# Kernel optimization log

Hardware: AMD Instinct MI355X
Metric: run time of the kernel (lower is better)

The kernel has to match this reference:

```python
import jax, jax.numpy as jnp
import numpy as np

B_, L_, D_MODEL = 4, 2048, 1024
D_STATE, EXPAND, D_CONV = 16, 2, 4
D_INNER = EXPAND * D_MODEL          # 2048
DT_RANK = (D_MODEL + 15) // 16      # 64 (mamba default: ceil(d_model/16))
EPS = 1e-6


def setup_inputs() -> dict:
    key = jax.random.key(0)
    ks = jax.random.split(key, 12)
    s = 0.02
    x = jax.random.normal(ks[0], (B_, L_, D_MODEL), dtype=jnp.float32)
    c = jax.random.normal(ks[1], (B_, D_MODEL), dtype=jnp.float32)
    W_in = jax.random.normal(ks[2], (D_MODEL, 2 * D_INNER), dtype=jnp.float32) * s
    conv_w = jax.random.normal(ks[3], (D_INNER, D_CONV), dtype=jnp.float32) * s
    conv_b = jnp.zeros((D_INNER,), dtype=jnp.float32)
    W_xproj = jax.random.normal(ks[4], (D_INNER, DT_RANK + 2 * D_STATE), dtype=jnp.float32) * s
    W_dt = jax.random.normal(ks[5], (DT_RANK, D_INNER), dtype=jnp.float32) * s
    # dt bias so softplus(dt) starts in a reasonable range (~0.001..0.1)
    dt = jnp.exp(jax.random.uniform(ks[6], (D_INNER,)) * (np.log(0.1) - np.log(0.001)) + np.log(0.001))
    b_dt = (dt + jnp.log(-jnp.expm1(-dt))).astype(jnp.float32)  # inverse softplus
    # A = repeat(1..d_state) per channel (mamba S4D-real init)
    A_log = jnp.log(jnp.tile(jnp.arange(1, D_STATE + 1, dtype=jnp.float32)[None, :], (D_INNER, 1)))
    D_skip = jnp.ones((D_INNER,), dtype=jnp.float32)
    W_out = jax.random.normal(ks[7], (D_INNER, D_MODEL), dtype=jnp.float32) * s
    W_ada = jax.random.normal(ks[8], (D_MODEL, 3 * D_MODEL), dtype=jnp.float32) * s
    b_ada = jnp.zeros((3 * D_MODEL,), dtype=jnp.float32)
    return dict(x=x, c=c, W_in=W_in, conv_w=conv_w, conv_b=conv_b,
                W_xproj=W_xproj, W_dt=W_dt, b_dt=b_dt, A_log=A_log,
                D_skip=D_skip, W_out=W_out, W_ada=W_ada, b_ada=b_ada)


def _mamba(x, W_in, conv_w, conv_b, W_xproj, W_dt, b_dt, A_log, D_skip, W_out):
    Bb, L, _ = x.shape
    xm, z = jnp.split(x @ W_in, 2, axis=-1)            # each [B, L, d_inner]
    # causal depthwise conv, kernel D_CONV
    xp = jnp.pad(xm, ((0, 0), (D_CONV - 1, 0), (0, 0)))
    xc = conv_b + sum(xp[:, k:k + L, :] * conv_w[:, k] for k in range(D_CONV))
    xc = jax.nn.silu(xc)                               # u: [B, L, d_inner]
    dbc = xc @ W_xproj
    dt, Bs, Cs = jnp.split(dbc, [DT_RANK, DT_RANK + D_STATE], axis=-1)
    delta = jax.nn.softplus(dt @ W_dt + b_dt)          # [B, L, d_inner]
    A = -jnp.exp(A_log)                                # [d_inner, d_state]

    def step(h, inp):
        d_t, B_t, C_t, u_t = inp                       # [B,di], [B,s], [B,s], [B,di]
        dA = jnp.exp(d_t[..., None] * A)               # [B, di, s]
        h = dA * h + (d_t * u_t)[..., None] * B_t[:, None, :]
        y = jnp.einsum('bds,bs->bd', h, C_t)
        return h, y

    xs = (jnp.moveaxis(delta, 1, 0), jnp.moveaxis(Bs, 1, 0),
          jnp.moveaxis(Cs, 1, 0), jnp.moveaxis(xc, 1, 0))
    h0 = jnp.zeros((Bb, D_INNER, D_STATE), dtype=x.dtype)
    _, ys = jax.lax.scan(step, h0, xs)
    y = jnp.moveaxis(ys, 0, 1) + xc * D_skip
    y = y * jax.nn.silu(z)
    return y @ W_out


def reference(x, c, W_in, conv_w, conv_b, W_xproj, W_dt, b_dt, A_log, D_skip, W_out, W_ada, b_ada):
    mod = jax.nn.silu(c) @ W_ada + b_ada
    scale, shift, gate = jnp.split(mod, 3, axis=-1)    # each [B, d_model]
    residual = x
    mu = x.mean(-1, keepdims=True)
    var = x.var(-1, keepdims=True)
    xn = (x - mu) * jax.lax.rsqrt(var + EPS)           # LayerNorm, no affine
    h = xn * (1.0 + scale[:, None, :]) + shift[:, None, :]
    out = _mamba(h, W_in, conv_w, conv_b, W_xproj, W_dt, b_dt, A_log, D_skip, W_out)
    return residual + gate[:, None, :] * out
```

## Files before the change

### kernel.cpp

```cpp
#include <hip/hip_runtime.h>
#include <hip/hip_bf16.h>
#include <stdint.h>


#define L_ 2048
#define DM 1024
#define DI 2048
#define DS 16
#define NC 32
#define TC 64

typedef __bf16 bf16x8 __attribute__((ext_vector_type(8)));
typedef float f32x4 __attribute__((ext_vector_type(4)));

__device__ __forceinline__ float bf2f(unsigned int u) {
  union { unsigned int i; float f; } c;
  c.i = (u & 0xFFFFu) << 16;
  return c.f;
}
__device__ __forceinline__ unsigned short f2bf(float f) {
  union { float f; unsigned int i; } c; c.f = f;
  unsigned int x = c.i;
  return (unsigned short)((x + 0x7FFFu + ((x >> 16) & 1u)) >> 16);
}
__device__ __forceinline__ float silu_f(float v) { return v / (1.f + __expf(-v)); }

__device__ __forceinline__ void async_cp16(unsigned short* lds, const unsigned short* g) {
  __builtin_amdgcn_global_load_lds(
      (const __attribute__((address_space(1))) unsigned int*)g,
      (__attribute__((address_space(3))) unsigned int*)lds, 16, 0, 0);
}

__global__ __launch_bounds__(256) void k_wt4(const float* __restrict__ s0, unsigned short* __restrict__ d0,
                                             const float* __restrict__ s1, unsigned short* __restrict__ d1,
                                             const float* __restrict__ s2, unsigned short* __restrict__ d2,
                                             const float* __restrict__ s3, unsigned short* __restrict__ d3) {
  int bid = blockIdx.x;
  const float* src; unsigned short* dst; int K, N, NP, kb, nb;
  if (bid < 4096)                { src = s0; dst = d0; K = 1024; N = 4096; NP = 4096; kb = bid & 31; nb = bid >> 5; }
  else if ((bid -= 4096) < 2048) { src = s1; dst = d1; K = 2048; N = 1024; NP = 1024; kb = bid & 63; nb = bid >> 6; }
  else if ((bid -= 2048) < 256)  { src = s2; dst = d2; K = 2048; N = 96;   NP = 128;  kb = bid & 63; nb = bid >> 6; }
  else { bid -= 256;               src = s3; dst = d3; K = 64;   N = 2048; NP = 2048; kb = bid & 1;  nb = bid >> 1; }
  __shared__ float tile[32][33];
  const int kb0 = kb * 32, nb0 = nb * 32;
  const int tx = threadIdx.x & 31, ty = threadIdx.x >> 5;
#pragma unroll
  for (int i = 0; i < 4; i++) {
    int k = kb0 + ty + 8 * i, n = nb0 + tx;
    float v = 0.f;
    if (k < K && n < N) v = src[(size_t)k * N + n];
    tile[ty + 8 * i][tx] = v;
  }
  __syncthreads();
#pragma unroll
  for (int i = 0; i < 4; i++) {
    int n = nb0 + ty + 8 * i, k = kb0 + tx;
    if (n < NP && k < K) dst[(size_t)n * K + k] = f2bf(tile[tx][ty + 8 * i]);
  }
}

__global__ __launch_bounds__(256) void k_ada(const float* __restrict__ c,
                                             const float* __restrict__ W,
                                             const float* __restrict__ bias,
                                             float* __restrict__ mod) {
  __shared__ float sc[DM];
  const int b = blockIdx.y, tid = threadIdx.x;
  for (int k = tid; k < DM; k += 256) sc[k] = silu_f(c[b * DM + k]);
  __syncthreads();
  const int j = blockIdx.x * 256 + tid;
  float acc = bias[j];
#pragma unroll 8
  for (int k = 0; k < DM; k++) acc += sc[k] * W[(size_t)k * 3072 + j];
  mod[b * 3072 + j] = acc;
}

__global__ __launch_bounds__(256) void k_ln(const float* __restrict__ x,
                                            const float* __restrict__ mod,
                                            unsigned short* __restrict__ h) {
  const int row = blockIdx.x, b = row >> 11, tid = threadIdx.x;
  const float4 v = ((const float4*)(x + (size_t)row * DM))[tid];
  float s = v.x + v.y + v.z + v.w;
  float ss = v.x * v.x + v.y * v.y + v.z * v.z + v.w * v.w;
#pragma unroll
  for (int off = 32; off; off >>= 1) { s += __shfl_down(s, off); ss += __shfl_down(ss, off); }
  __shared__ float red[10];
  const int wv = tid >> 6, ln = tid & 63;
  if (ln == 0) { red[wv] = s; red[4 + wv] = ss; }
  __syncthreads();
  if (tid == 0) {
    float st = red[0] + red[1] + red[2] + red[3];
    float sst = red[4] + red[5] + red[6] + red[7];
    float mu = st * (1.f / DM);
    red[8] = mu;
    red[9] = rsqrtf(sst * (1.f / DM) - mu * mu + 1e-6f);
  }
  __syncthreads();
  const float mu = red[8], rstd = red[9];
  const int ccol = tid * 4;
  const float4 sc = *(const float4*)(mod + b * 3072 + ccol);
  const float4 sh = *(const float4*)(mod + b * 3072 + DM + ccol);
  uint2 p;
  p.x = (unsigned)f2bf((v.x - mu) * rstd * (1.f + sc.x) + sh.x) |
        ((unsigned)f2bf((v.y - mu) * rstd * (1.f + sc.y) + sh.y) << 16);
  p.y = (unsigned)f2bf((v.z - mu) * rstd * (1.f + sc.z) + sh.z) |
        ((unsigned)f2bf((v.w - mu) * rstd * (1.f + sc.w) + sh.w) << 16);
  *(uint2*)(h + (size_t)row * DM + ccol) = p;
}

struct GArgs {
  const unsigned short* A;
  const unsigned short* Bt;
  int lda, ldb, klen;
  float* f0;
  unsigned short* h0;
  unsigned short* h1;
  const float* c0;
  const float* c1;
};

template<int EPI>
__global__ __launch_bounds__(256, 2) void k_gemm(GArgs g) {
  __shared__ unsigned short sA[128 * 32];
  __shared__ unsigned short sB[128 * 32];
  const int tid = threadIdx.x;
  const int w = tid >> 6, lane = tid & 63;
  const int m0 = blockIdx.x * 128, n0 = blockIdx.y * 128;
  const int kstart = blockIdx.z * g.klen;
  const int r4 = lane >> 2;
  const int c8 = (lane & 3) * 8;
  const int rowA0 = w * 16 + r4, rowA1 = (w + 4) * 16 + r4;
  const unsigned short* gA0 = g.A + (size_t)(m0 + rowA0) * g.lda + kstart + c8;
  const unsigned short* gA1 = g.A + (size_t)(m0 + rowA1) * g.lda + kstart + c8;
  const unsigned short* gB0 = g.Bt + (size_t)(n0 + rowA0) * g.ldb + kstart + c8;
  const unsigned short* gB1 = g.Bt + (size_t)(n0 + rowA1) * g.ldb + kstart + c8;
  unsigned short* lA0 = sA + w * 512;
  unsigned short* lA1 = sA + (w + 4) * 512;
  unsigned short* lB0 = sB + w * 512;
  unsigned short* lB1 = sB + (w + 4) * 512;
  const int mw = (w & 1) * 64, nw = (w >> 1) * 64;
  const int row16 = lane & 15, k8 = (lane >> 4) * 8;
  f32x4 acc[4][4] = {};
  for (int kk = 0; kk < g.klen; kk += 32) {
    async_cp16(lA0, gA0); async_cp16(lA1, gA1);
    async_cp16(lB0, gB0); async_cp16(lB1, gB1);
    gA0 += 32; gA1 += 32; gB0 += 32; gB1 += 32;
    __syncthreads();
    bf16x8 av[4], bv[4];
#pragma unroll
    for (int i = 0; i < 4; i++)
      av[i] = *(const bf16x8*)(sA + (mw + 16 * i + row16) * 32 + k8);
#pragma unroll
    for (int j = 0; j < 4; j++)
      bv[j] = *(const bf16x8*)(sB + (nw + 16 * j + row16) * 32 + k8);
#pragma unroll
    for (int i = 0; i < 4; i++)
#pragma unroll
      for (int j = 0; j < 4; j++)
        acc[i][j] = __builtin_amdgcn_mfma_f32_16x16x32_bf16(av[i], bv[j], acc[i][j], 0, 0, 0);
    __syncthreads();
  }
  const int qr = (lane >> 4) * 4, cn = lane & 15;
#pragma unroll
  for (int i = 0; i < 4; i++) {
    const int m = m0 + mw + 16 * i + qr;
    const int b = m >> 11;
#pragma unroll
    for (int j = 0; j < 4; j++) {
      const int n = n0 + nw + 16 * j + cn;
      f32x4 v = acc[i][j];
      if constexpr (EPI == 0) {
#pragma unroll
        for (int r = 0; r < 4; r++) {
          unsigned short* dst = (n < DI)
              ? g.h0 + (size_t)(m + r) * DI + n
              : g.h1 + (size_t)(m + r) * DI + (n - DI);
          *dst = f2bf(v[r]);
        }
      } else if constexpr (EPI == 1) {
        *(f32x4*)(g.f0 + ((size_t)(blockIdx.z * 128 + n)) * 8192 + m) = v;
      } else if constexpr (EPI == 2) {
        const float bn = g.c0[n];
#pragma unroll
        for (int r = 0; r < 4; r++) {
          float xx = v[r] + bn;
          g.h0[(size_t)(m + r) * DI + n] = f2bf((xx > 15.f) ? xx : __logf(1.f + __expf(xx)));
        }
      } else {
        const float gate = g.c1[b * 3072 + 2048 + n];
#pragma unroll
        for (int r = 0; r < 4; r++) {
          size_t idx = (size_t)(m + r) * DM + n;
          g.f0[idx] = g.c0[idx] + gate * v[r];
        }
      }
    }
  }
}

__global__ __launch_bounds__(256) void k_conv(const unsigned short* __restrict__ xm,
                                              const float* __restrict__ conv_w,
                                              const float* __restrict__ conv_b,
                                              unsigned short* __restrict__ u) {
  const int b = blockIdx.z;
  const int t = blockIdx.x * 32 + (threadIdx.x >> 3);
  const int d = blockIdx.y * 64 + (threadIdx.x & 7) * 8;
  const size_t rowbase = ((size_t)(b * L_ + t)) * DI + d;
  uint4 r3 = *(const uint4*)(xm + rowbase);
  uint4 r0 = make_uint4(0, 0, 0, 0), r1 = r0, r2 = r0;
  if (t >= 3) r0 = *(const uint4*)(xm + rowbase - 3 * DI);
  if (t >= 2) r1 = *(const uint4*)(xm + rowbase - 2 * DI);
  if (t >= 1) r2 = *(const uint4*)(xm + rowbase - 1 * DI);
  float x0[8], x1[8], x2[8], x3[8];
  const unsigned* p0 = (const unsigned*)&r0;
  const unsigned* p1 = (const unsigned*)&r1;
  const unsigned* p2 = (const unsigned*)&r2;
  const unsigned* p3 = (const unsigned*)&r3;
#pragma unroll
  for (int q = 0; q < 4; q++) {
    x0[2 * q] = bf2f(p0[q]); x0[2 * q + 1] = bf2f(p0[q] >> 16);
    x1[2 * q] = bf2f(p1[q]); x1[2 * q + 1] = bf2f(p1[q] >> 16);
    x2[2 * q] = bf2f(p2[q]); x2[2 * q + 1] = bf2f(p2[q] >> 16);
    x3[2 * q] = bf2f(p3[q]); x3[2 * q + 1] = bf2f(p3[q] >> 16);
  }
  const f32x4 cb0 = *(const f32x4*)(conv_b + d);
  const f32x4 cb1 = *(const f32x4*)(conv_b + d + 4);
  unsigned out[4];
#pragma unroll
  for (int j = 0; j < 8; j++) {
    const f32x4 wj = *(const f32x4*)(conv_w + (size_t)(d + j) * 4);
    const float cb = (j < 4) ? cb0[j] : cb1[j - 4];
    float a = cb + wj[0] * x0[j] + wj[1] * x1[j] + wj[2] * x2[j] + wj[3] * x3[j];
    unsigned short us = f2bf(silu_f(a));
    if (j & 1) out[j >> 1] |= ((unsigned)us << 16);
    else out[j >> 1] = us;
  }
  *(uint4*)(u + rowbase) = make_uint4(out[0], out[1], out[2], out[3]);
}

__global__ __launch_bounds__(256) void k_xsplit(const float* __restrict__ pt,
                                                unsigned short* __restrict__ dtb,
                                                float* __restrict__ BC) {
  const int bx = blockIdx.x;
  const int n = bx >> 5;
  const int m = ((bx & 31) << 8) + threadIdx.x;
  float v = pt[(size_t)n * 8192 + m] + pt[(size_t)(128 + n) * 8192 + m] +
            pt[(size_t)(256 + n) * 8192 + m] + pt[(size_t)(384 + n) * 8192 + m];
  if (n < 64) dtb[(size_t)m * 64 + n] = f2bf(v);
  else if (n < 80) BC[(size_t)m * 32 + (n - 64)] = v;
  else BC[(size_t)m * 32 + 16 + (n - 80)] = v;
}

__global__ __launch_bounds__(256, 4) void k_scanA(const unsigned short* __restrict__ delta,
                                                  const unsigned short* __restrict__ u,
                                                  const float* __restrict__ BC,
                                                  const float* __restrict__ A_log,
                                                  float* __restrict__ hloc,
                                                  float* __restrict__ dsum) {
  const int b = blockIdx.y, c = blockIdx.z;
  const int d = blockIdx.x * 256 + threadIdx.x;
  const size_t mbase = (size_t)(b * L_ + c * TC);
  const unsigned short* dp = delta + mbase * DI + d;
  const unsigned short* up = u + mbase * DI + d;
  const float* bc = BC + mbase * 32;
  float As[16];
#pragma unroll
  for (int q = 0; q < 4; q++) {
    const f32x4 av = *(const f32x4*)(A_log + (size_t)d * 16 + q * 4);
#pragma unroll
    for (int j = 0; j < 4; j++) As[q * 4 + j] = -__expf(av[j]);
  }
  float h[16];
#pragma unroll
  for (int s = 0; s < 16; s++) h[s] = 0.f;
  float sd = 0.f;
  for (int t8 = 0; t8 < TC; t8 += 8) {
    float dv[8], uvf[8];
#pragma unroll
    for (int i = 0; i < 8; i++) dv[i] = bf2f(dp[(size_t)(t8 + i) * DI]);
#pragma unroll
    for (int i = 0; i < 8; i++) uvf[i] = bf2f(up[(size_t)(t8 + i) * DI]);
#pragma unroll
    for (int i = 0; i < 8; i++) {
      const float dvi = dv[i];
      const float w = dvi * uvf[i];
      sd += dvi;
      const float* bct = bc + (size_t)(t8 + i) * 32;
#pragma unroll
      for (int q = 0; q < 4; q++) {
        const f32x4 bq = *(const f32x4*)(bct + q * 4);
#pragma unroll
        for (int j = 0; j < 4; j++) {
          const int s = q * 4 + j;
          const float a = __expf(dvi * As[s]);
          h[s] = a * h[s] + w * bq[j];
        }
      }
    }
  }
  float* hl = hloc + (((size_t)(b * NC + c)) * DI + d) * 16;
#pragma unroll
  for (int q = 0; q < 4; q++) {
    f32x4 v = {h[q * 4], h[q * 4 + 1], h[q * 4 + 2], h[q * 4 + 3]};
    *(f32x4*)(hl + q * 4) = v;
  }
  dsum[((size_t)(b * NC + c)) * DI + d] = sd;
}

__global__ __launch_bounds__(256) void k_scanB(const float* __restrict__ hloc,
                                               const float* __restrict__ dsum,
                                               const float* __restrict__ A_log,
                                               float* __restrict__ hin) {
  const int i = blockIdx.x * 256 + threadIdx.x;
  const int b = i >> 11, d = i & 2047;
  float As[16];
#pragma unroll
  for (int q = 0; q < 4; q++) {
    const f32x4 av = *(const f32x4*)(A_log + (size_t)d * 16 + q * 4);
#pragma unroll
    for (int j = 0; j < 4; j++) As[q * 4 + j] = -__expf(av[j]);
  }
  float H[16];
#pragma unroll
  for (int s = 0; s < 16; s++) H[s] = 0.f;
  for (int c = 0; c < NC; c++) {
    float* hp = hin + (((size_t)(b * NC + c)) * DI + d) * 16;
#pragma unroll
    for (int q = 0; q < 4; q++) {
      f32x4 v = {H[q * 4], H[q * 4 + 1], H[q * 4 + 2], H[q * 4 + 3]};
      *(f32x4*)(hp + q * 4) = v;
    }
    if (c < NC - 1) {
      const float sd = dsum[((size_t)(b * NC + c)) * DI + d];
      const float* hl = hloc + (((size_t)(b * NC + c)) * DI + d) * 16;
#pragma unroll
      for (int s = 0; s < 16; s++)
        H[s] = __expf(sd * As[s]) * H[s] + hl[s];
    }
  }
}

__global__ __launch_bounds__(256, 4) void k_scanC(const unsigned short* __restrict__ delta,
                                                  const unsigned short* __restrict__ u,
                                                  const unsigned short* __restrict__ z,
                                                  const float* __restrict__ BC,
                                                  const float* __restrict__ A_log,
                                                  const float* __restrict__ Dsk,
                                                  const float* __restrict__ hin,
                                                  unsigned short* __restrict__ y) {
  const int b = blockIdx.y, c = blockIdx.z;
  const int d = blockIdx.x * 256 + threadIdx.x;
  const size_t mbase = (size_t)(b * L_ + c * TC);
  const unsigned short* dp = delta + mbase * DI + d;
  const unsigned short* up = u + mbase * DI + d;
  const unsigned short* zp = z + mbase * DI + d;
  const float* bc = BC + mbase * 32;
  float As[16];
#pragma unroll
  for (int q = 0; q < 4; q++) {
    const f32x4 av = *(const f32x4*)(A_log + (size_t)d * 16 + q * 4);
#pragma unroll
    for (int j = 0; j < 4; j++) As[q * 4 + j] = -__expf(av[j]);
  }
  const float dsk = Dsk[d];
  float h[16];
  const float* hp = hin + (((size_t)(b * NC + c)) * DI + d) * 16;
#pragma unroll
  for (int q = 0; q < 4; q++) {
    const f32x4 v = *(const f32x4*)(hp + q * 4);
#pragma unroll
    for (int j = 0; j < 4; j++) h[q * 4 + j] = v[j];
  }
  unsigned short* yp = y + mbase * DI + d;
  for (int t8 = 0; t8 < TC; t8 += 8) {
    float dv[8], uvf[8], zvf[8];
#pragma unroll
    for (int i = 0; i < 8; i++) dv[i] = bf2f(dp[(size_t)(t8 + i) * DI]);
#pragma unroll
    for (int i = 0; i < 8; i++) uvf[i] = bf2f(up[(size_t)(t8 + i) * DI]);
#pragma unroll
    for (int i = 0; i < 8; i++) zvf[i] = bf2f(zp[(size_t)(t8 + i) * DI]);
#pragma unroll
    for (int i = 0; i < 8; i++) {
      const float dvi = dv[i];
      const float w = dvi * uvf[i];
      const float* bct = bc + (size_t)(t8 + i) * 32;
      float y0 = 0.f, y1 = 0.f;
#pragma unroll
      for (int q = 0; q < 4; q++) {
        const f32x4 bq = *(const f32x4*)(bct + q * 4);
        const f32x4 cq = *(const f32x4*)(bct + 16 + q * 4);
#pragma unroll
        for (int j = 0; j < 4; j++) {
          const int s = q * 4 + j;
          const float a = __expf(dvi * As[s]);
          h[s] = a * h[s] + w * bq[j];
          if (j & 1) y1 += h[s] * cq[j]; else y0 += h[s] * cq[j];
        }
      }
      const float yt = (y0 + y1 + uvf[i] * dsk) * silu_f(zvf[i]);
      yp[(size_t)(t8 + i) * DI] = f2bf(yt);
    }
  }
}

extern "C" void kernel_launch(void* const* d_in, const int* in_sizes, int n_in,
                              void* d_out, int out_size, void* d_ws, size_t ws_size,
                              hipStream_t stream) {
  const float* x      = (const float*)d_in[0];
  const float* c      = (const float*)d_in[1];
  const float* W_in   = (const float*)d_in[2];
  const float* conv_w = (const float*)d_in[3];
  const float* conv_b = (const float*)d_in[4];
  const float* W_xp   = (const float*)d_in[5];
  const float* W_dt   = (const float*)d_in[6];
  const float* b_dt   = (const float*)d_in[7];
  const float* A_log  = (const float*)d_in[8];
  const float* D_skip = (const float*)d_in[9];
  const float* W_out  = (const float*)d_in[10];
  const float* W_ada  = (const float*)d_in[11];
  const float* b_ada  = (const float*)d_in[12];
  float* out = (float*)d_out;

  char* ws = (char*)d_ws;
  size_t off = 0;
  auto take = [&](size_t bytes) {
    char* p = ws + off;
    off += (bytes + 255) & ~(size_t)255;
    return p;
  };
  float* mod             = (float*)take((size_t)4 * 3072 * 4);
  unsigned short* Wt_in  = (unsigned short*)take((size_t)4096 * 1024 * 2);
  unsigned short* Wt_out = (unsigned short*)take((size_t)1024 * 2048 * 2);
  unsigned short* Wt_xp  = (unsigned short*)take((size_t)128 * 2048 * 2);
  unsigned short* Wt_dt  = (unsigned short*)take((size_t)2048 * 64 * 2);
  unsigned short* h_bf   = (unsigned short*)take((size_t)8192 * 1024 * 2);
  unsigned short* xm     = (unsigned short*)take((size_t)4 * 2048 * 2048 * 2);
  unsigned short* z_bf   = (unsigned short*)take((size_t)4 * 2048 * 2048 * 2);
  unsigned short* scanws = (unsigned short*)take((size_t)4 * 2048 * 2048 * 2);
  unsigned short* u_bf   = (unsigned short*)take((size_t)8192 * 2048 * 2);
  unsigned short* delta  = (unsigned short*)take((size_t)8192 * 2048 * 2);
  unsigned short* dt_bf  = (unsigned short*)take((size_t)8192 * 64 * 2);
  float* BC              = (float*)take((size_t)4 * 2048 * 32 * 4);
  float* part_T = (float*)h_bf;
  float* hin    = (float*)h_bf;
  float* hloc   = (float*)scanws;
  float* dsum   = (float*)(scanws + (size_t)8 * 1024 * 1024);
  unsigned short* y_bf = xm;

  k_wt4<<<6528, 256, 0, stream>>>(W_in, Wt_in, W_out, Wt_out, W_xp, Wt_xp, W_dt, Wt_dt);
  k_ada<<<dim3(12, 4), 256, 0, stream>>>(c, W_ada, b_ada, mod);
  k_ln<<<8192, 256, 0, stream>>>(x, mod, h_bf);
  GArgs a1{h_bf, Wt_in, 1024, 1024, 1024, nullptr, xm, z_bf, nullptr, nullptr};
  k_gemm<0><<<dim3(64, 32), 256, 0, stream>>>(a1);
  k_conv<<<dim3(64, 32, 4), 256, 0, stream>>>(xm, conv_w, conv_b, u_bf);
  GArgs a2{u_bf, Wt_xp, 2048, 2048, 512, part_T, nullptr, nullptr, nullptr, nullptr};
  k_gemm<1><<<dim3(64, 1, 4), 256, 0, stream>>>(a2);
  k_xsplit<<<3072, 256, 0, stream>>>(part_T, dt_bf, BC);
  GArgs a3{dt_bf, Wt_dt, 64, 64, 64, nullptr, delta, nullptr, b_dt, nullptr};
  k_gemm<2><<<dim3(64, 16), 256, 0, stream>>>(a3);
  k_scanA<<<dim3(8, 4, NC - 1), 256, 0, stream>>>(delta, u_bf, BC, A_log, hloc, dsum);
  k_scanB<<<32, 256, 0, stream>>>(hloc, dsum, A_log, hin);
  k_scanC<<<dim3(8, 4, NC), 256, 0, stream>>>(delta, u_bf, z_bf, BC, A_log, D_skip, hin, y_bf);
  GArgs a4{y_bf, Wt_out, 2048, 2048, 2048, out, nullptr, nullptr, x, mod};
  k_gemm<3><<<dim3(64, 8), 256, 0, stream>>>(a4);
}
```

Measured before the change: 587.5 us.

## Replace per-state exps in scan with a power chain when A is arithmetic

```diff
diff --git a/kernel.cpp b/kernel.cpp
--- a/kernel.cpp
+++ b/kernel.cpp
@@ -25,25 +25,66 @@
 }
 __device__ __forceinline__ float silu_f(float v) { return v / (1.f + __expf(-v)); }
 
+__device__ __forceinline__ void pow_chain(float a1, float* p) {
+  p[0] = a1;
+#pragma unroll
+  for (int s = 1; s < 16; s++) p[s] = p[(s - 1) >> 1] * p[s >> 1];
+}
+
 __device__ __forceinline__ void async_cp16(unsigned short* lds, const unsigned short* g) {
   __builtin_amdgcn_global_load_lds(
       (const __attribute__((address_space(1))) unsigned int*)g,
       (__attribute__((address_space(3))) unsigned int*)lds, 16, 0, 0);
 }
 
-__global__ __launch_bounds__(256) void k_wt4(const float* __restrict__ s0, unsigned short* __restrict__ d0,
+__global__ __launch_bounds__(256) void k_chk(const float* __restrict__ A_log,
+                                             int* __restrict__ flag) {
+  __shared__ int ok;
+  if (threadIdx.x == 0) ok = 1;
+  __syncthreads();
+  int good = 1;
+  for (int i = threadIdx.x; i < DI * DS; i += 256) {
+    const int s = i & 15, d = i >> 4;
+    const float a = __expf(A_log[i]);
+    const float expect = __expf(A_log[d * 16]) * (float)(s + 1);
+    if (fabsf(a - expect) > 1e-4f * expect) good = 0;
+  }
+  if (!good) atomicAnd(&ok, 0);
+  __syncthreads();
+  if (threadIdx.x == 0) flag[0] = ok;
+}
+
+__global__ __launch_bounds__(256) void k_pre(const float* __restrict__ s0, unsigned short* __restrict__ d0,
                                              const float* __restrict__ s1, unsigned short* __restrict__ d1,
                                              const float* __restrict__ s2, unsigned short* __restrict__ d2,
-                                             const float* __restrict__ s3, unsigned short* __restrict__ d3) {
+                                             const float* __restrict__ s3, unsigned short* __restrict__ d3,
+                                             const float* __restrict__ cvec,
+                                             const float* __restrict__ W_ada,
+                                             const float* __restrict__ b_ada,
+                                             float* __restrict__ mod) {
+  __shared__ float tile[32][33];
   int bid = blockIdx.x;
+  const int tid = threadIdx.x;
+  if (bid >= 6528) {
+    bid -= 6528;
+    const int b = bid / 12, jb = bid % 12;
+    float* sc = &tile[0][0];
+    for (int k = tid; k < DM; k += 256) sc[k] = silu_f(cvec[b * DM + k]);
+    __syncthreads();
+    const int j = jb * 256 + tid;
+    float acc = b_ada[j];
+#pragma unroll 8
+    for (int k = 0; k < DM; k++) acc += sc[k] * W_ada[(size_t)k * 3072 + j];
+    mod[b * 3072 + j] = acc;
+    return;
+  }
   const float* src; unsigned short* dst; int K, N, NP, kb, nb;
   if (bid < 4096)                { src = s0; dst = d0; K = 1024; N = 4096; NP = 4096; kb = bid & 31; nb = bid >> 5; }
   else if ((bid -= 4096) < 2048) { src = s1; dst = d1; K = 2048; N = 1024; NP = 1024; kb = bid & 63; nb = bid >> 6; }
   else if ((bid -= 2048) < 256)  { src = s2; dst = d2; K = 2048; N = 96;   NP = 128;  kb = bid & 63; nb = bid >> 6; }
   else { bid -= 256;               src = s3; dst = d3; K = 64;   N = 2048; NP = 2048; kb = bid & 1;  nb = bid >> 1; }
-  __shared__ float tile[32][33];
   const int kb0 = kb * 32, nb0 = nb * 32;
-  const int tx = threadIdx.x & 31, ty = threadIdx.x >> 5;
+  const int tx = tid & 31, ty = tid >> 5;
 #pragma unroll
   for (int i = 0; i < 4; i++) {
     int k = kb0 + ty + 8 * i, n = nb0 + tx;
@@ -57,21 +98,6 @@
     int n = nb0 + ty + 8 * i, k = kb0 + tx;
     if (n < NP && k < K) dst[(size_t)n * K + k] = f2bf(tile[tx][ty + 8 * i]);
   }
-}
-
-__global__ __launch_bounds__(256) void k_ada(const float* __restrict__ c,
-                                             const float* __restrict__ W,
-                                             const float* __restrict__ bias,
-                                             float* __restrict__ mod) {
-  __shared__ float sc[DM];
-  const int b = blockIdx.y, tid = threadIdx.x;
-  for (int k = tid; k < DM; k += 256) sc[k] = silu_f(c[b * DM + k]);
-  __syncthreads();
-  const int j = blockIdx.x * 256 + tid;
-  float acc = bias[j];
-#pragma unroll 8
-  for (int k = 0; k < DM; k++) acc += sc[k] * W[(size_t)k * 3072 + j];
-  mod[b * 3072 + j] = acc;
 }
 
 __global__ __launch_bounds__(256) void k_ln(const float* __restrict__ x,
@@ -254,45 +280,75 @@
                                                   const unsigned short* __restrict__ u,
                                                   const float* __restrict__ BC,
                                                   const float* __restrict__ A_log,
+                                                  const int* __restrict__ flag,
                                                   float* __restrict__ hloc,
                                                   float* __restrict__ dsum) {
   const int b = blockIdx.y, c = blockIdx.z;
   const int d = blockIdx.x * 256 + threadIdx.x;
+  const int fast = flag[0];
   const size_t mbase = (size_t)(b * L_ + c * TC);
   const unsigned short* dp = delta + mbase * DI + d;
   const unsigned short* up = u + mbase * DI + d;
   const float* bc = BC + mbase * 32;
-  float As[16];
-#pragma unroll
-  for (int q = 0; q < 4; q++) {
-    const f32x4 av = *(const f32x4*)(A_log + (size_t)d * 16 + q * 4);
-#pragma unroll
-    for (int j = 0; j < 4; j++) As[q * 4 + j] = -__expf(av[j]);
-  }
   float h[16];
 #pragma unroll
   for (int s = 0; s < 16; s++) h[s] = 0.f;
   float sd = 0.f;
-  for (int t8 = 0; t8 < TC; t8 += 8) {
-    float dv[8], uvf[8];
-#pragma unroll
-    for (int i = 0; i < 8; i++) dv[i] = bf2f(dp[(size_t)(t8 + i) * DI]);
-#pragma unroll
-    for (int i = 0; i < 8; i++) uvf[i] = bf2f(up[(size_t)(t8 + i) * DI]);
-#pragma unroll
-    for (int i = 0; i < 8; i++) {
-      const float dvi = dv[i];
-      const float w = dvi * uvf[i];
-      sd += dvi;
-      const float* bct = bc + (size_t)(t8 + i) * 32;
-#pragma unroll
-      for (int q = 0; q < 4; q++) {
-        const f32x4 bq = *(const f32x4*)(bct + q * 4);
-#pragma unroll
-        for (int j = 0; j < 4; j++) {
-          const int s = q * 4 + j;
-          const float a = __expf(dvi * As[s]);
-          h[s] = a * h[s] + w * bq[j];
+  if (fast) {
+    const float As0 = -__expf(A_log[(size_t)d * 16]);
+    for (int t8 = 0; t8 < TC; t8 += 8) {
+      float dv[8], uvf[8];
+#pragma unroll
+      for (int i = 0; i < 8; i++) dv[i] = bf2f(dp[(size_t)(t8 + i) * DI]);
+#pragma unroll
+      for (int i = 0; i < 8; i++) uvf[i] = bf2f(up[(size_t)(t8 + i) * DI]);
+#pragma unroll
+      for (int i = 0; i < 8; i++) {
+        const float dvi = dv[i];
+        const float w = dvi * uvf[i];
+        sd += dvi;
+        const float* bct = bc + (size_t)(t8 + i) * 32;
+        float p[16];
+        pow_chain(__expf(dvi * As0), p);
+#pragma unroll
+        for (int q = 0; q < 4; q++) {
+          const f32x4 bq = *(const f32x4*)(bct + q * 4);
+#pragma unroll
+          for (int j = 0; j < 4; j++) {
+            const int s = q * 4 + j;
+            h[s] = p[s] * h[s] + w * bq[j];
+          }
+        }
+      }
+    }
+  } else {
+    float As[16];
+#pragma unroll
+    for (int q = 0; q < 4; q++) {
+      const f32x4 av = *(const f32x4*)(A_log + (size_t)d * 16 + q * 4);
+#pragma unroll
+      for (int j = 0; j < 4; j++) As[q * 4 + j] = -__expf(av[j]);
+    }
+    for (int t8 = 0; t8 < TC; t8 += 8) {
+      float dv[8], uvf[8];
+#pragma unroll
+      for (int i = 0; i < 8; i++) dv[i] = bf2f(dp[(size_t)(t8 + i) * DI]);
+#pragma unroll
+      for (int i = 0; i < 8; i++) uvf[i] = bf2f(up[(size_t)(t8 + i) * DI]);
+#pragma unroll
+      for (int i = 0; i < 8; i++) {
+        const float dvi = dv[i];
+        const float w = dvi * uvf[i];
+        sd += dvi;
+        const float* bct = bc + (size_t)(t8 + i) * 32;
+#pragma unroll
+        for (int q = 0; q < 4; q++) {
+          const f32x4 bq = *(const f32x4*)(bct + q * 4);
+#pragma unroll
+          for (int j = 0; j < 4; j++) {
+            const int s = q * 4 + j;
+            h[s] = __expf(dvi * As[s]) * h[s] + w * bq[j];
+          }
         }
       }
     }
@@ -309,15 +365,20 @@
 __global__ __launch_bounds__(256) void k_scanB(const float* __restrict__ hloc,
                                                const float* __restrict__ dsum,
                                                const float* __restrict__ A_log,
+                                               const int* __restrict__ flag,
                                                float* __restrict__ hin) {
   const int i = blockIdx.x * 256 + threadIdx.x;
   const int b = i >> 11, d = i & 2047;
+  const int fast = flag[0];
   float As[16];
-#pragma unroll
-  for (int q = 0; q < 4; q++) {
-    const f32x4 av = *(const f32x4*)(A_log + (size_t)d * 16 + q * 4);
-#pragma unroll
-    for (int j = 0; j < 4; j++) As[q * 4 + j] = -__expf(av[j]);
+  const float As0 = -__expf(A_log[(size_t)d * 16]);
+  if (!fast) {
+#pragma unroll
+    for (int q = 0; q < 4; q++) {
+      const f32x4 av = *(const f32x4*)(A_log + (size_t)d * 16 + q * 4);
+#pragma unroll
+      for (int j = 0; j < 4; j++) As[q * 4 + j] = -__expf(av[j]);
+    }
   }
   float H[16];
 #pragma unroll
@@ -332,9 +393,15 @@
     if (c < NC - 1) {
       const float sd = dsum[((size_t)(b * NC + c)) * DI + d];
       const float* hl = hloc + (((size_t)(b * NC + c)) * DI + d) * 16;
-#pragma unroll
-      for (int s = 0; s < 16; s++)
-        H[s] = __expf(sd * As[s]) * H[s] + hl[s];
+      if (fast) {
+        float p[16];
+        pow_chain(__expf(sd * As0), p);
+#pragma unroll
+        for (int s = 0; s < 16; s++) H[s] = p[s] * H[s] + hl[s];
+      } else {
+#pragma unroll
+        for (int s = 0; s < 16; s++) H[s] = __expf(sd * As[s]) * H[s] + hl[s];
+      }
     }
   }
 }
@@ -345,22 +412,17 @@
                                                   const float* __restrict__ BC,
                                                   const float* __restrict__ A_log,
                                                   const float* __restrict__ Dsk,
+                                                  const int* __restrict__ flag,
                                                   const float* __restrict__ hin,
                                                   unsigned short* __restrict__ y) {
   const int b = blockIdx.y, c = blockIdx.z;
   const int d = blockIdx.x * 256 + threadIdx.x;
+  const int fast = flag[0];
   const size_t mbase = (size_t)(b * L_ + c * TC);
   const unsigned short* dp = delta + mbase * DI + d;
   const unsigned short* up = u + mbase * DI + d;
   const unsigned short* zp = z + mbase * DI + d;
   const float* bc = BC + mbase * 32;
-  float As[16];
-#pragma unroll
-  for (int q = 0; q < 4; q++) {
-    const f32x4 av = *(const f32x4*)(A_log + (size_t)d * 16 + q * 4);
-#pragma unroll
-    for (int j = 0; j < 4; j++) As[q * 4 + j] = -__expf(av[j]);
-  }
   const float dsk = Dsk[d];
   float h[16];
   const float* hp = hin + (((size_t)(b * NC + c)) * DI + d) * 16;
@@ -371,34 +433,75 @@
     for (int j = 0; j < 4; j++) h[q * 4 + j] = v[j];
   }
   unsigned short* yp = y + mbase * DI + d;
-  for (int t8 = 0; t8 < TC; t8 += 8) {
-    float dv[8], uvf[8], zvf[8];
-#pragma unroll
-    for (int i = 0; i < 8; i++) dv[i] = bf2f(dp[(size_t)(t8 + i) * DI]);
-#pragma unroll
-    for (int i = 0; i < 8; i++) uvf[i] = bf2f(up[(size_t)(t8 + i) * DI]);
-#pragma unroll
-    for (int i = 0; i < 8; i++) zvf[i] = bf2f(zp[(size_t)(t8 + i) * DI]);
-#pragma unroll
-    for (int i = 0; i < 8; i++) {
-      const float dvi = dv[i];
-      const float w = dvi * uvf[i];
-      const float* bct = bc + (size_t)(t8 + i) * 32;
-      float y0 = 0.f, y1 = 0.f;
-#pragma unroll
-      for (int q = 0; q < 4; q++) {
-        const f32x4 bq = *(const f32x4*)(bct + q * 4);
-        const f32x4 cq = *(const f32x4*)(bct + 16 + q * 4);
-#pragma unroll
-        for (int j = 0; j < 4; j++) {
-          const int s = q * 4 + j;
-          const float a = __expf(dvi * As[s]);
-          h[s] = a * h[s] + w * bq[j];
-          if (j & 1) y1 += h[s] * cq[j]; else y0 += h[s] * cq[j];
-        }
+  if (fast) {
+    const float As0 = -__expf(A_log[(size_t)d * 16]);
+    for (int t8 = 0; t8 < TC; t8 += 8) {
+      float dv[8], uvf[8], zvf[8];
+#pragma unroll
+      for (int i = 0; i < 8; i++) dv[i] = bf2f(dp[(size_t)(t8 + i) * DI]);
+#pragma unroll
+      for (int i = 0; i < 8; i++) uvf[i] = bf2f(up[(size_t)(t8 + i) * DI]);
+#pragma unroll
+      for (int i = 0; i < 8; i++) zvf[i] = bf2f(zp[(size_t)(t8 + i) * DI]);
+#pragma unroll
+      for (int i = 0; i < 8; i++) {
+        const float dvi = dv[i];
+        const float w = dvi * uvf[i];
+        const float* bct = bc + (size_t)(t8 + i) * 32;
+        float p[16];
+        pow_chain(__expf(dvi * As0), p);
+        float y0 = 0.f, y1 = 0.f;
+#pragma unroll
+        for (int q = 0; q < 4; q++) {
+          const f32x4 bq = *(const f32x4*)(bct + q * 4);
+          const f32x4 cq = *(const f32x4*)(bct + 16 + q * 4);
+#pragma unroll
+          for (int j = 0; j < 4; j++) {
+            const int s = q * 4 + j;
+            h[s] = p[s] * h[s] + w * bq[j];
+            if (j & 1) y1 += h[s] * cq[j]; else y0 += h[s] * cq[j];
+          }
+        }
+        const float yt = (y0 + y1 + uvf[i] * dsk) * silu_f(zvf[i]);
+        yp[(size_t)(t8 + i) * DI] = f2bf(yt);
       }
-      const float yt = (y0 + y1 + uvf[i] * dsk) * silu_f(zvf[i]);
-      yp[(size_t)(t8 + i) * DI] = f2bf(yt);
+    }
+  } else {
+    float As[16];
+#pragma unroll
+    for (int q = 0; q < 4; q++) {
+      const f32x4 av = *(const f32x4*)(A_log + (size_t)d * 16 + q * 4);
+#pragma unroll
+      for (int j = 0; j < 4; j++) As[q * 4 + j] = -__expf(av[j]);
+    }
+    for (int t8 = 0; t8 < TC; t8 += 8) {
+      float dv[8], uvf[8], zvf[8];
+#pragma unroll
+      for (int i = 0; i < 8; i++) dv[i] = bf2f(dp[(size_t)(t8 + i) * DI]);
+#pragma unroll
+      for (int i = 0; i < 8; i++) uvf[i] = bf2f(up[(size_t)(t8 + i) * DI]);
+#pragma unroll
+      for (int i = 0; i < 8; i++) zvf[i] = bf2f(zp[(size_t)(t8 + i) * DI]);
+#pragma unroll
+      for (int i = 0; i < 8; i++) {
+        const float dvi = dv[i];
+        const float w = dvi * uvf[i];
+        const float* bct = bc + (size_t)(t8 + i) * 32;
+        float y0 = 0.f, y1 = 0.f;
+#pragma unroll
+        for (int q = 0; q < 4; q++) {
+          const f32x4 bq = *(const f32x4*)(bct + q * 4);
+          const f32x4 cq = *(const f32x4*)(bct + 16 + q * 4);
+#pragma unroll
+          for (int j = 0; j < 4; j++) {
+            const int s = q * 4 + j;
+            h[s] = __expf(dvi * As[s]) * h[s] + w * bq[j];
+            if (j & 1) y1 += h[s] * cq[j]; else y0 += h[s] * cq[j];
+          }
+        }
+        const float yt = (y0 + y1 + uvf[i] * dsk) * silu_f(zvf[i]);
+        yp[(size_t)(t8 + i) * DI] = f2bf(yt);
+      }
     }
   }
 }
@@ -441,14 +544,16 @@
   unsigned short* delta  = (unsigned short*)take((size_t)8192 * 2048 * 2);
   unsigned short* dt_bf  = (unsigned short*)take((size_t)8192 * 64 * 2);
   float* BC              = (float*)take((size_t)4 * 2048 * 32 * 4);
+  int* flag              = (int*)take(256);
   float* part_T = (float*)h_bf;
   float* hin    = (float*)h_bf;
   float* hloc   = (float*)scanws;
   float* dsum   = (float*)(scanws + (size_t)8 * 1024 * 1024);
   unsigned short* y_bf = xm;
 
-  k_wt4<<<6528, 256, 0, stream>>>(W_in, Wt_in, W_out, Wt_out, W_xp, Wt_xp, W_dt, Wt_dt);
-  k_ada<<<dim3(12, 4), 256, 0, stream>>>(c, W_ada, b_ada, mod);
+  k_chk<<<1, 256, 0, stream>>>(A_log, flag);
+  k_pre<<<6576, 256, 0, stream>>>(W_in, Wt_in, W_out, Wt_out, W_xp, Wt_xp, W_dt, Wt_dt,
+                                  c, W_ada, b_ada, mod);
   k_ln<<<8192, 256, 0, stream>>>(x, mod, h_bf);
   GArgs a1{h_bf, Wt_in, 1024, 1024, 1024, nullptr, xm, z_bf, nullptr, nullptr};
   k_gemm<0><<<dim3(64, 32), 256, 0, stream>>>(a1);
@@ -458,9 +563,9 @@
   k_xsplit<<<3072, 256, 0, stream>>>(part_T, dt_bf, BC);
   GArgs a3{dt_bf, Wt_dt, 64, 64, 64, nullptr, delta, nullptr, b_dt, nullptr};
   k_gemm<2><<<dim3(64, 16), 256, 0, stream>>>(a3);
-  k_scanA<<<dim3(8, 4, NC - 1), 256, 0, stream>>>(delta, u_bf, BC, A_log, hloc, dsum);
-  k_scanB<<<32, 256, 0, stream>>>(hloc, dsum, A_log, hin);
-  k_scanC<<<dim3(8, 4, NC), 256, 0, stream>>>(delta, u_bf, z_bf, BC, A_log, D_skip, hin, y_bf);
+  k_scanA<<<dim3(8, 4, NC - 1), 256, 0, stream>>>(delta, u_bf, BC, A_log, flag, hloc, dsum);
+  k_scanB<<<32, 256, 0, stream>>>(hloc, dsum, A_log, flag, hin);
+  k_scanC<<<dim3(8, 4, NC), 256, 0, stream>>>(delta, u_bf, z_bf, BC, A_log, D_skip, flag, hin, y_bf);
   GArgs a4{y_bf, Wt_out, 2048, 2048, 2048, out, nullptr, nullptr, x, mod};
   k_gemm<3><<<dim3(64, 8), 256, 0, stream>>>(a4);
 }
```

After: 714.5 us. 21.6% more time.
